# Optimization experiments

Hardware: AMD Instinct MI355X
Metric: run time of the kernel (lower is better)

Reference implementation:

```python
import jax, jax.numpy as jnp
import numpy as np

B, C, H, W, K, NH = 4, 128, 64, 64, 7, 8
DH = C // NH          # per-head dim
PAD = (K - 1) // 2    # symmetric padding since K is odd


def setup_inputs() -> dict:
    key = jax.random.key(0)
    ks = jax.random.split(key, 9)
    s = 1.0 / np.sqrt(C)
    f32 = jnp.float32
    return {
        "x": jax.random.normal(ks[0], (B, C, H, W), f32),
        "wq": jax.random.normal(ks[1], (C, C), f32) * s,
        "bq": jax.random.normal(ks[2], (C,), f32) * 0.01,
        "wk": jax.random.normal(ks[3], (C, C), f32) * s,
        "bk": jax.random.normal(ks[4], (C,), f32) * 0.01,
        "wv": jax.random.normal(ks[5], (C, C), f32) * s,
        "bv": jax.random.normal(ks[6], (C,), f32) * 0.01,
        "pos_h": jax.random.normal(ks[7], (NH, K), f32) * 0.02,
        "pos_w": jax.random.normal(ks[8], (NH, K), f32) * 0.02,
    }


def _unfold(p):
    # p: [B,C,H+K-1,W+K-1] -> [B,C,H,W,K,K] (KxK neighborhood per pixel),
    # matching torch .unfold(2,K,1).unfold(3,K,1). Loop is over fixed kernel size only.
    p1 = jnp.stack([p[:, :, i:i + H, :] for i in range(K)], axis=-1)      # [B,C,H,W+K-1,K]
    return jnp.stack([p1[:, :, :, j:j + W, :] for j in range(K)], axis=-1)  # [B,C,H,W,K,K]


def reference(x, wq, bq, wk, bk, wv, bv, pos_h, pos_w):
    cx = x  # cx defaults to x in the original module
    pc = jnp.pad(cx, ((0, 0), (0, 0), (PAD, PAD), (PAD, PAD)))
    # 1x1 convs are pointwise channel mixes
    k = jnp.einsum('oc,bchw->bohw', wk, pc) + bk[None, :, None, None]
    v = jnp.einsum('oc,bchw->bohw', wv, pc) + bv[None, :, None, None]
    q = jnp.einsum('oc,bchw->bohw', wq, x) + bq[None, :, None, None]

    ku = _unfold(k).reshape(B, NH, DH, H, W, K, K)
    vu = _unfold(v).reshape(B, NH, DH, H, W, K, K)
    qh = q.reshape(B, NH, DH, H, W)

    # per-pixel logits over KxK neighborhood
    logits = jnp.einsum('bndhw,bndhwij->bnhwij', qh, ku)  # [B,NH,H,W,K,K]
    logits = logits + pos_h[None, :, None, None, :, None] + pos_w[None, :, None, None, None, :]

    weights = jax.nn.softmax(logits.reshape(B, NH, H, W, K * K), axis=-1)
    out = jnp.einsum('bnhwk,bndhwk->bndhw', weights, vu.reshape(B, NH, DH, H, W, K * K))
    return out.reshape(B, C, H, W)
```

## Files before the change

### kernel.cpp

```cpp
#include <hip/hip_runtime.h>
#include <cmath>

constexpr int Bn = 4, Cn = 128, Hn = 64, Wn = 64, Kn = 7, NHn = 8, DHn = 16, PADn = 3;
constexpr int HWn = Hn * Wn;
constexpr int TS = 16;
constexpr int HALO = TS + Kn - 1;
constexpr int NPIX = HALO * HALO;
constexpr int PSTRIDE_U16 = 24;
constexpr int PSTRIDE_U32 = 12;

typedef float f32x4 __attribute__((ext_vector_type(4)));
typedef short short8 __attribute__((ext_vector_type(8)));
typedef unsigned int u32x4 __attribute__((ext_vector_type(4)));
typedef unsigned short u16x4 __attribute__((ext_vector_type(4)));
typedef unsigned short u16x8 __attribute__((ext_vector_type(8)));

__device__ __forceinline__ unsigned short f32_to_bf16_rne(float f) {
  unsigned u = __float_as_uint(f);
  unsigned r = u + 0x7fffu + ((u >> 16) & 1u);
  return (unsigned short)(r >> 16);
}
__device__ __forceinline__ float bf16_to_f32(unsigned short h) {
  return __uint_as_float(((unsigned)h) << 16);
}
__device__ __forceinline__ float bflo(unsigned u) { return __uint_as_float(u << 16); }
__device__ __forceinline__ float bfhi(unsigned u) { return __uint_as_float(u & 0xffff0000u); }

__global__ __launch_bounds__(256)
void prep(const float* __restrict__ x,
          const float* __restrict__ wq, const float* __restrict__ wk,
          const float* __restrict__ wv,
          unsigned short* __restrict__ Whl, unsigned short* __restrict__ xThl)
{
  const int t = threadIdx.x;
  if (blockIdx.z == 4) {
    if (blockIdx.y != 0 || blockIdx.x >= 48) return;
    const int mat = blockIdx.x >> 4;
    const int chunk = blockIdx.x & 15;
    const float* W = (mat == 0) ? wq : (mat == 1) ? wk : wv;
    const int i = (chunk * 256 + t) * 4;
    const f32x4 v = *reinterpret_cast<const f32x4*>(W + i);
    unsigned short h[4], l[4];
#pragma unroll
    for (int j = 0; j < 4; ++j) {
      h[j] = f32_to_bf16_rne(v[j]);
      l[j] = f32_to_bf16_rne(v[j] - bf16_to_f32(h[j]));
    }
    unsigned short* base = Whl + (size_t)mat * 2 * 16384;
    *reinterpret_cast<uint2*>(base + i) =
        make_uint2(h[0] | ((unsigned)h[1] << 16), h[2] | ((unsigned)h[3] << 16));
    *reinterpret_cast<uint2*>(base + 16384 + i) =
        make_uint2(l[0] | ((unsigned)l[1] << 16), l[2] | ((unsigned)l[3] << 16));
    return;
  }

  __shared__ float sm[32][65];
  const int b   = blockIdx.z;
  const int c0g = blockIdx.y * 32;
  const int p0g = blockIdx.x * 64;
  const float* xb = x + (size_t)b * Cn * HWn;

#pragma unroll
  for (int rep = 0; rep < 2; ++rep) {
    const int cl = rep * 16 + (t >> 4);
    const int pl = (t & 15) * 4;
    const f32x4 v = *reinterpret_cast<const f32x4*>(xb + (size_t)(c0g + cl) * HWn + p0g + pl);
    sm[cl][pl + 0] = v[0]; sm[cl][pl + 1] = v[1];
    sm[cl][pl + 2] = v[2]; sm[cl][pl + 3] = v[3];
  }
  __syncthreads();

  const int pl = t >> 2;
  const int c0 = (t & 3) * 8;
  u32x4 hw, lw;
#pragma unroll
  for (int j = 0; j < 4; ++j) {
    const float v0 = sm[c0 + 2 * j][pl];
    const float v1 = sm[c0 + 2 * j + 1][pl];
    const unsigned short h0 = f32_to_bf16_rne(v0);
    const unsigned short h1 = f32_to_bf16_rne(v1);
    const unsigned short l0 = f32_to_bf16_rne(v0 - bf16_to_f32(h0));
    const unsigned short l1 = f32_to_bf16_rne(v1 - bf16_to_f32(h1));
    hw[j] = h0 | ((unsigned)h1 << 16);
    lw[j] = l0 | ((unsigned)l1 << 16);
  }
  unsigned short* dst = xThl + (size_t)b * 2 * HWn * Cn + (size_t)(p0g + pl) * Cn + c0g + c0;
  *reinterpret_cast<u32x4*>(dst)            = hw;
  *reinterpret_cast<u32x4*>(dst + HWn * Cn) = lw;
}

__global__ __launch_bounds__(64)
void qkv_mfma(const unsigned short* __restrict__ Whl,
              const unsigned short* __restrict__ xThl,
              const float* __restrict__ bq_, const float* __restrict__ bk_,
              const float* __restrict__ bv_,
              float* __restrict__ qo, unsigned short* __restrict__ kbf,
              unsigned short* __restrict__ vbf)
{
  const int z   = blockIdx.z;
  const int mat = z >> 2;
  const int b   = z & 3;
  const float* bias = (mat == 0) ? bq_ : (mat == 1) ? bk_ : bv_;

  const int lane = threadIdx.x;
  const int r    = lane & 15;
  const int quad = lane >> 4;
  const int mbase = blockIdx.y * 64;
  const int nbase = blockIdx.x * 64;

  const unsigned short* Wm = Whl  + (size_t)mat * 2 * Cn * Cn;
  const unsigned short* Xb = xThl + (size_t)b   * 2 * HWn * Cn;

  f32x4 acc[4][4] = {};

#pragma unroll
  for (int ks = 0; ks < 4; ++ks) {
    const int kk = ks * 32 + quad * 8;
    short8 Ah[4], Al[4], Bh[4], Bl[4];
#pragma unroll
    for (int mt = 0; mt < 4; ++mt) {
      const unsigned short* p = Wm + (size_t)(mbase + mt * 16 + r) * Cn + kk;
      Ah[mt] = *reinterpret_cast<const short8*>(p);
      Al[mt] = *reinterpret_cast<const short8*>(p + Cn * Cn);
    }
#pragma unroll
    for (int nt = 0; nt < 4; ++nt) {
      const unsigned short* p = Xb + (size_t)(nbase + nt * 16 + r) * Cn + kk;
      Bh[nt] = *reinterpret_cast<const short8*>(p);
      Bl[nt] = *reinterpret_cast<const short8*>(p + HWn * Cn);
    }
#pragma unroll
    for (int mt = 0; mt < 4; ++mt)
#pragma unroll
      for (int nt = 0; nt < 4; ++nt) {
        acc[mt][nt] = __builtin_amdgcn_mfma_f32_16x16x32_bf16(Ah[mt], Bh[nt], acc[mt][nt], 0, 0, 0);
        acc[mt][nt] = __builtin_amdgcn_mfma_f32_16x16x32_bf16(Ah[mt], Bl[nt], acc[mt][nt], 0, 0, 0);
        acc[mt][nt] = __builtin_amdgcn_mfma_f32_16x16x32_bf16(Al[mt], Bh[nt], acc[mt][nt], 0, 0, 0);
      }
  }

#pragma unroll
  for (int mt = 0; mt < 4; ++mt) {
    const int n = blockIdx.y * 4 + mt;
    const f32x4 b4 = *reinterpret_cast<const f32x4*>(bias + mbase + mt * 16 + quad * 4);
#pragma unroll
    for (int nt = 0; nt < 4; ++nt) {
      const int p = nbase + nt * 16 + r;
      const size_t off = ((size_t)((b * NHn + n) * HWn + p)) * DHn + quad * 4;
      f32x4 val = acc[mt][nt] + b4;
      if (mat == 0) {
        *reinterpret_cast<f32x4*>(qo + off) = val;
      } else {
        unsigned short* y = (mat == 1) ? kbf : vbf;
        u16x4 pk;
        pk[0] = f32_to_bf16_rne(val[0]); pk[1] = f32_to_bf16_rne(val[1]);
        pk[2] = f32_to_bf16_rne(val[2]); pk[3] = f32_to_bf16_rne(val[3]);
        *reinterpret_cast<u16x4*>(y + off) = pk;
      }
    }
  }
}

__global__ __launch_bounds__(256)
void sasa_attn(const float* __restrict__ q, const unsigned short* __restrict__ kbf,
               const unsigned short* __restrict__ vbf, const float* __restrict__ bk_,
               const float* __restrict__ bv_, const float* __restrict__ pos_h,
               const float* __restrict__ pos_w, float* __restrict__ out)
{
  __shared__ __align__(16) unsigned short ksm[NPIX * PSTRIDE_U16];
  __shared__ __align__(16) unsigned short vsm[NPIX * PSTRIDE_U16];

  const int z  = blockIdx.z;
  const int b  = z >> 3;
  const int n  = z & 7;
  const int h0 = blockIdx.y * TS;
  const int w0 = blockIdx.x * TS;
  const int tid = threadIdx.x;
  const int tx = tid & 15;
  const int ty = tid >> 4;
  const int cbase = n * DHn;

  const unsigned short* kb = kbf + ((size_t)(b * NHn + n) * HWn) * DHn;
  const unsigned short* vb = vbf + ((size_t)(b * NHn + n) * HWn) * DHn;

  u16x8 kb0, kb1, vb0, vb1;
#pragma unroll
  for (int j = 0; j < 8; ++j) {
    kb0[j] = f32_to_bf16_rne(bk_[cbase + j]);
    kb1[j] = f32_to_bf16_rne(bk_[cbase + 8 + j]);
    vb0[j] = f32_to_bf16_rne(bv_[cbase + j]);
    vb1[j] = f32_to_bf16_rne(bv_[cbase + 8 + j]);
  }

  for (int c = tid; c < NPIX * 2; c += 256) {
    const int pix  = c >> 1;
    const int half = c & 1;
    const int hh = pix / HALO;
    const int ww = pix - hh * HALO;
    const int gh = h0 + hh - PADn;
    const int gw = w0 + ww - PADn;
    const bool inb = (gh >= 0) && (gh < Hn) && (gw >= 0) && (gw < Wn);
    u16x8 kd, vd;
    if (inb) {
      const size_t src = ((size_t)(gh * Wn + gw)) * DHn + half * 8;
      kd = *reinterpret_cast<const u16x8*>(kb + src);
      vd = *reinterpret_cast<const u16x8*>(vb + src);
    } else {
      kd = half ? kb1 : kb0;
      vd = half ? vb1 : vb0;
    }
    const int dst = pix * PSTRIDE_U16 + half * 8;
    *reinterpret_cast<u16x8*>(ksm + dst) = kd;
    *reinterpret_cast<u16x8*>(vsm + dst) = vd;
  }

  const int h = h0 + ty, w = w0 + tx;
  const int p = h * Wn + w;
  const float* qp = q + ((size_t)(b * NHn + n) * HWn + p) * DHn;
  float qr[DHn];
#pragma unroll
  for (int j = 0; j < 4; ++j) {
    const f32x4 t4 = *reinterpret_cast<const f32x4*>(qp + j * 4);
    qr[j * 4 + 0] = t4[0]; qr[j * 4 + 1] = t4[1];
    qr[j * 4 + 2] = t4[2]; qr[j * 4 + 3] = t4[3];
  }

  __syncthreads();

  const unsigned* ksu = reinterpret_cast<const unsigned*>(ksm);
  const unsigned* vsu = reinterpret_cast<const unsigned*>(vsm);

  float logits[Kn * Kn];
#pragma unroll
  for (int i = 0; i < Kn; ++i) {
    const float ph = pos_h[n * Kn + i];
#pragma unroll
    for (int j = 0; j < Kn; ++j) {
      const int base = ((ty + i) * HALO + (tx + j)) * PSTRIDE_U32;
      const u32x4 a = *reinterpret_cast<const u32x4*>(ksu + base);
      const u32x4 c = *reinterpret_cast<const u32x4*>(ksu + base + 4);
      float acc = qr[0] * bflo(a[0]);
      acc = fmaf(qr[1],  bfhi(a[0]), acc);
      acc = fmaf(qr[2],  bflo(a[1]), acc);  acc = fmaf(qr[3],  bfhi(a[1]), acc);
      acc = fmaf(qr[4],  bflo(a[2]), acc);  acc = fmaf(qr[5],  bfhi(a[2]), acc);
      acc = fmaf(qr[6],  bflo(a[3]), acc);  acc = fmaf(qr[7],  bfhi(a[3]), acc);
      acc = fmaf(qr[8],  bflo(c[0]), acc);  acc = fmaf(qr[9],  bfhi(c[0]), acc);
      acc = fmaf(qr[10], bflo(c[1]), acc);  acc = fmaf(qr[11], bfhi(c[1]), acc);
      acc = fmaf(qr[12], bflo(c[2]), acc);  acc = fmaf(qr[13], bfhi(c[2]), acc);
      acc = fmaf(qr[14], bflo(c[3]), acc);  acc = fmaf(qr[15], bfhi(c[3]), acc);
      logits[i * Kn + j] = acc + ph + pos_w[n * Kn + j];
    }
  }

  float mx = -1e30f;
#pragma unroll
  for (int t = 0; t < Kn * Kn; ++t) mx = fmaxf(mx, logits[t]);
  float sum = 0.0f;
#pragma unroll
  for (int t = 0; t < Kn * Kn; ++t) {
    const float e = __expf(logits[t] - mx);
    logits[t] = e;
    sum += e;
  }
  const float inv = 1.0f / sum;

  float o[DHn] = {};
#pragma unroll
  for (int i = 0; i < Kn; ++i) {
#pragma unroll
    for (int j = 0; j < Kn; ++j) {
      const float wt = logits[i * Kn + j];
      const int base = ((ty + i) * HALO + (tx + j)) * PSTRIDE_U32;
      const u32x4 a = *reinterpret_cast<const u32x4*>(vsu + base);
      const u32x4 c = *reinterpret_cast<const u32x4*>(vsu + base + 4);
      o[0]  = fmaf(wt, bflo(a[0]), o[0]);   o[1]  = fmaf(wt, bfhi(a[0]), o[1]);
      o[2]  = fmaf(wt, bflo(a[1]), o[2]);   o[3]  = fmaf(wt, bfhi(a[1]), o[3]);
      o[4]  = fmaf(wt, bflo(a[2]), o[4]);   o[5]  = fmaf(wt, bfhi(a[2]), o[5]);
      o[6]  = fmaf(wt, bflo(a[3]), o[6]);   o[7]  = fmaf(wt, bfhi(a[3]), o[7]);
      o[8]  = fmaf(wt, bflo(c[0]), o[8]);   o[9]  = fmaf(wt, bfhi(c[0]), o[9]);
      o[10] = fmaf(wt, bflo(c[1]), o[10]);  o[11] = fmaf(wt, bfhi(c[1]), o[11]);
      o[12] = fmaf(wt, bflo(c[2]), o[12]);  o[13] = fmaf(wt, bfhi(c[2]), o[13]);
      o[14] = fmaf(wt, bflo(c[3]), o[14]);  o[15] = fmaf(wt, bfhi(c[3]), o[15]);
    }
  }

  float* ob = out + ((size_t)(b * Cn + cbase)) * HWn + p;
#pragma unroll
  for (int d = 0; d < DHn; ++d) ob[(size_t)d * HWn] = o[d] * inv;
}

extern "C" void kernel_launch(void* const* d_in, const int* in_sizes, int n_in,
                              void* d_out, int out_size, void* d_ws, size_t ws_size,
                              hipStream_t stream) {
  const float* x     = (const float*)d_in[0];
  const float* wq    = (const float*)d_in[1];
  const float* bq    = (const float*)d_in[2];
  const float* wk    = (const float*)d_in[3];
  const float* bk    = (const float*)d_in[4];
  const float* wv    = (const float*)d_in[5];
  const float* bv    = (const float*)d_in[6];
  const float* pos_h = (const float*)d_in[7];
  const float* pos_w = (const float*)d_in[8];
  float* out = (float*)d_out;

  const size_t tensor_elems = (size_t)Bn * Cn * HWn;
  float*          q    = (float*)d_ws;
  unsigned short* kbf  = (unsigned short*)(q + tensor_elems);
  unsigned short* vbf  = kbf + tensor_elems;
  unsigned short* Whl  = vbf + tensor_elems;
  unsigned short* xThl = Whl + (size_t)3 * 2 * Cn * Cn;

  dim3 gp(HWn / 64, Cn / 32, Bn + 1);
  prep<<<gp, 256, 0, stream>>>(x, wq, wk, wv, Whl, xThl);

  dim3 g1(HWn / 64, Cn / 64, 3 * Bn);
  qkv_mfma<<<g1, 64, 0, stream>>>(Whl, xThl, bq, bk, bv, q, kbf, vbf);

  dim3 g2(Wn / TS, Hn / TS, Bn * NHn);
  sasa_attn<<<g2, 256, 0, stream>>>(q, kbf, vbf, bk, bv, pos_h, pos_w, out);
}
```

Measured before the change: 111.5 us.

## Compute neighborhood attention logits and weighted sum with MFMA instructions

Rewrites the attention kernel so each wavefront processes a 16-pixel row segment and computes the 7x7 neighborhood logits and the value aggregation with bf16 16x16x32 MFMA, using a banded 16-wide window with masked positional bias. Q is now stored as split bf16 hi/lo planes so the MFMA dot product keeps near-fp32 query precision, and V is transposed into a channel-major packed LDS layout to act as the B operand. This replaces many scalar FMAs per pixel with matrix instructions, at the cost of redundant work on masked window entries and bf16 rounding of the softmax weights.

```diff
diff --git a/kernel.cpp b/kernel.cpp
--- a/kernel.cpp
+++ b/kernel.cpp
@@ -4,10 +4,12 @@
 constexpr int Bn = 4, Cn = 128, Hn = 64, Wn = 64, Kn = 7, NHn = 8, DHn = 16, PADn = 3;
 constexpr int HWn = Hn * Wn;
 constexpr int TS = 16;
-constexpr int HALO = TS + Kn - 1;
-constexpr int NPIX = HALO * HALO;
-constexpr int PSTRIDE_U16 = 24;
-constexpr int PSTRIDE_U32 = 12;
+constexpr size_t QPLANE = (size_t)Bn * NHn * HWn * DHn;
+
+constexpr int HR = 22;
+constexpr int HC = 24;
+constexpr int KP = 24;
+constexpr int VW = 14;
 
 typedef float f32x4 __attribute__((ext_vector_type(4)));
 typedef short short8 __attribute__((ext_vector_type(8)));
@@ -23,8 +25,16 @@
 __device__ __forceinline__ float bf16_to_f32(unsigned short h) {
   return __uint_as_float(((unsigned)h) << 16);
 }
-__device__ __forceinline__ float bflo(unsigned u) { return __uint_as_float(u << 16); }
-__device__ __forceinline__ float bfhi(unsigned u) { return __uint_as_float(u & 0xffff0000u); }
+__device__ __forceinline__ unsigned pk_bf16(float lo, float hi) {
+  return (__float_as_uint(lo) >> 16) | (__float_as_uint(hi) & 0xffff0000u);
+}
+__device__ __forceinline__ f32x4 max4(f32x4 a, f32x4 b) {
+  a[0] = fmaxf(a[0], b[0]); a[1] = fmaxf(a[1], b[1]);
+  a[2] = fmaxf(a[2], b[2]); a[3] = fmaxf(a[3], b[3]);
+  return a;
+}
+
+union UVcast { u32x4 u; short8 s; };
 
 __global__ __launch_bounds__(256)
 void prep(const float* __restrict__ x,
@@ -94,7 +104,7 @@
               const unsigned short* __restrict__ xThl,
               const float* __restrict__ bq_, const float* __restrict__ bk_,
               const float* __restrict__ bv_,
-              float* __restrict__ qo, unsigned short* __restrict__ kbf,
+              unsigned short* __restrict__ qo, unsigned short* __restrict__ kbf,
               unsigned short* __restrict__ vbf)
 {
   const int z   = blockIdx.z;
@@ -149,39 +159,54 @@
       const size_t off = ((size_t)((b * NHn + n) * HWn + p)) * DHn + quad * 4;
       f32x4 val = acc[mt][nt] + b4;
       if (mat == 0) {
-        *reinterpret_cast<f32x4*>(qo + off) = val;
+        u16x4 hi4, lo4;
+#pragma unroll
+        for (int j = 0; j < 4; ++j) {
+          const unsigned short hb = f32_to_bf16_rne(val[j]);
+          hi4[j] = hb;
+          lo4[j] = f32_to_bf16_rne(val[j] - bf16_to_f32(hb));
+        }
+        *reinterpret_cast<u16x4*>(qo + off)          = hi4;
+        *reinterpret_cast<u16x4*>(qo + QPLANE + off) = lo4;
       } else {
         unsigned short* y = (mat == 1) ? kbf : vbf;
-        u16x4 pk;
-        pk[0] = f32_to_bf16_rne(val[0]); pk[1] = f32_to_bf16_rne(val[1]);
-        pk[2] = f32_to_bf16_rne(val[2]); pk[3] = f32_to_bf16_rne(val[3]);
-        *reinterpret_cast<u16x4*>(y + off) = pk;
+        u16x4 pkv;
+        pkv[0] = f32_to_bf16_rne(val[0]); pkv[1] = f32_to_bf16_rne(val[1]);
+        pkv[2] = f32_to_bf16_rne(val[2]); pkv[3] = f32_to_bf16_rne(val[3]);
+        *reinterpret_cast<u16x4*>(y + off) = pkv;
       }
     }
   }
 }
 
 __global__ __launch_bounds__(256)
-void sasa_attn(const float* __restrict__ q, const unsigned short* __restrict__ kbf,
-               const unsigned short* __restrict__ vbf, const float* __restrict__ bk_,
-               const float* __restrict__ bv_, const float* __restrict__ pos_h,
-               const float* __restrict__ pos_w, float* __restrict__ out)
+void sasa_attn(const unsigned short* __restrict__ qhl,
+               const unsigned short* __restrict__ kbf,
+               const unsigned short* __restrict__ vbf,
+               const float* __restrict__ bk_, const float* __restrict__ bv_,
+               const float* __restrict__ pos_h, const float* __restrict__ pos_w,
+               float* __restrict__ out)
 {
-  __shared__ __align__(16) unsigned short ksm[NPIX * PSTRIDE_U16];
-  __shared__ __align__(16) unsigned short vsm[NPIX * PSTRIDE_U16];
+  __shared__ __align__(16) unsigned short ksm[HR * HC * KP];
+  __shared__ __align__(16) unsigned       vsm[HR * DHn * VW];
 
   const int z  = blockIdx.z;
   const int b  = z >> 3;
   const int n  = z & 7;
   const int h0 = blockIdx.y * TS;
   const int w0 = blockIdx.x * TS;
-  const int tid = threadIdx.x;
-  const int tx = tid & 15;
-  const int ty = tid >> 4;
+  const int tid  = threadIdx.x;
+  const int lane = tid & 63;
+  const int wv   = tid >> 6;
+  const int r    = lane & 15;
+  const int quad = lane >> 4;
   const int cbase = n * DHn;
 
   const unsigned short* kb = kbf + ((size_t)(b * NHn + n) * HWn) * DHn;
   const unsigned short* vb = vbf + ((size_t)(b * NHn + n) * HWn) * DHn;
+  const size_t qbase = ((size_t)(b * NHn + n) * HWn) * DHn;
+  const unsigned short* qhp = qhl + qbase;
+  const unsigned short* qlp = qhl + QPLANE + qbase;
 
   u16x8 kb0, kb1, vb0, vb1;
 #pragma unroll
@@ -192,101 +217,141 @@
     vb1[j] = f32_to_bf16_rne(bv_[cbase + 8 + j]);
   }
 
-  for (int c = tid; c < NPIX * 2; c += 256) {
+  for (int c = tid; c < HR * HC * 2; c += 256) {
     const int pix  = c >> 1;
     const int half = c & 1;
-    const int hh = pix / HALO;
-    const int ww = pix - hh * HALO;
+    const int hh = pix / HC;
+    const int ww = pix - hh * HC;
     const int gh = h0 + hh - PADn;
     const int gw = w0 + ww - PADn;
     const bool inb = (gh >= 0) && (gh < Hn) && (gw >= 0) && (gw < Wn);
-    u16x8 kd, vd;
-    if (inb) {
-      const size_t src = ((size_t)(gh * Wn + gw)) * DHn + half * 8;
-      kd = *reinterpret_cast<const u16x8*>(kb + src);
-      vd = *reinterpret_cast<const u16x8*>(vb + src);
-    } else {
-      kd = half ? kb1 : kb0;
-      vd = half ? vb1 : vb0;
-    }
-    const int dst = pix * PSTRIDE_U16 + half * 8;
-    *reinterpret_cast<u16x8*>(ksm + dst) = kd;
-    *reinterpret_cast<u16x8*>(vsm + dst) = vd;
-  }
-
-  const int h = h0 + ty, w = w0 + tx;
-  const int p = h * Wn + w;
-  const float* qp = q + ((size_t)(b * NHn + n) * HWn + p) * DHn;
-  float qr[DHn];
-#pragma unroll
-  for (int j = 0; j < 4; ++j) {
-    const f32x4 t4 = *reinterpret_cast<const f32x4*>(qp + j * 4);
-    qr[j * 4 + 0] = t4[0]; qr[j * 4 + 1] = t4[1];
-    qr[j * 4 + 2] = t4[2]; qr[j * 4 + 3] = t4[3];
+    u16x8 kd;
+    if (inb) kd = *reinterpret_cast<const u16x8*>(kb + ((size_t)(gh * Wn + gw)) * DHn + half * 8);
+    else     kd = half ? kb1 : kb0;
+    *reinterpret_cast<u16x8*>(ksm + pix * KP + half * 8) = kd;
+  }
+
+  for (int pp = tid; pp < HR * (HC / 2); pp += 256) {
+    const int hh = pp / (HC / 2);
+    const int wp = pp - hh * (HC / 2);
+    const int gh = h0 + hh - PADn;
+    u16x8 a0, a1, c0, c1;
+    {
+      const int gw = w0 + 2 * wp - PADn;
+      const bool inb = (gh >= 0) && (gh < Hn) && (gw >= 0) && (gw < Wn);
+      if (inb) {
+        const size_t src = ((size_t)(gh * Wn + gw)) * DHn;
+        a0 = *reinterpret_cast<const u16x8*>(vb + src);
+        a1 = *reinterpret_cast<const u16x8*>(vb + src + 8);
+      } else { a0 = vb0; a1 = vb1; }
+    }
+    {
+      const int gw = w0 + 2 * wp + 1 - PADn;
+      const bool inb = (gh >= 0) && (gh < Hn) && (gw >= 0) && (gw < Wn);
+      if (inb) {
+        const size_t src = ((size_t)(gh * Wn + gw)) * DHn;
+        c0 = *reinterpret_cast<const u16x8*>(vb + src);
+        c1 = *reinterpret_cast<const u16x8*>(vb + src + 8);
+      } else { c0 = vb0; c1 = vb1; }
+    }
+    unsigned* dst = vsm + (hh * DHn) * VW + wp;
+#pragma unroll
+    for (int d = 0; d < 8; ++d)
+      dst[d * VW] = (unsigned)(unsigned short)a0[d] | ((unsigned)(unsigned short)c0[d] << 16);
+#pragma unroll
+    for (int d = 0; d < 8; ++d)
+      dst[(8 + d) * VW] = (unsigned)(unsigned short)a1[d] | ((unsigned)(unsigned short)c1[d] << 16);
+  }
+
+  float ph[7];
+#pragma unroll
+  for (int i = 0; i < 7; ++i) ph[i] = pos_h[n * Kn + i];
+  f32x4 pw4[2];
+#pragma unroll
+  for (int win = 0; win < 2; ++win) {
+#pragma unroll
+    for (int reg = 0; reg < 4; ++reg) {
+      const int ww = win * 8 + 4 * quad + reg;
+      const int j  = ww - r;
+      const bool valid = (j >= 0) && (j < 7) && (win == 0 || ww >= 16);
+      const int jc = j < 0 ? 0 : (j > 6 ? 6 : j);
+      const float pv = pos_w[n * Kn + jc];
+      pw4[win][reg] = valid ? pv : -1e30f;
+    }
   }
 
   __syncthreads();
 
-  const unsigned* ksu = reinterpret_cast<const unsigned*>(ksm);
-  const unsigned* vsu = reinterpret_cast<const unsigned*>(vsm);
-
-  float logits[Kn * Kn];
-#pragma unroll
-  for (int i = 0; i < Kn; ++i) {
-    const float ph = pos_h[n * Kn + i];
-#pragma unroll
-    for (int j = 0; j < Kn; ++j) {
-      const int base = ((ty + i) * HALO + (tx + j)) * PSTRIDE_U32;
-      const u32x4 a = *reinterpret_cast<const u32x4*>(ksu + base);
-      const u32x4 c = *reinterpret_cast<const u32x4*>(ksu + base + 4);
-      float acc = qr[0] * bflo(a[0]);
-      acc = fmaf(qr[1],  bfhi(a[0]), acc);
-      acc = fmaf(qr[2],  bflo(a[1]), acc);  acc = fmaf(qr[3],  bfhi(a[1]), acc);
-      acc = fmaf(qr[4],  bflo(a[2]), acc);  acc = fmaf(qr[5],  bfhi(a[2]), acc);
-      acc = fmaf(qr[6],  bflo(a[3]), acc);  acc = fmaf(qr[7],  bfhi(a[3]), acc);
-      acc = fmaf(qr[8],  bflo(c[0]), acc);  acc = fmaf(qr[9],  bfhi(c[0]), acc);
-      acc = fmaf(qr[10], bflo(c[1]), acc);  acc = fmaf(qr[11], bfhi(c[1]), acc);
-      acc = fmaf(qr[12], bflo(c[2]), acc);  acc = fmaf(qr[13], bfhi(c[2]), acc);
-      acc = fmaf(qr[14], bflo(c[3]), acc);  acc = fmaf(qr[15], bfhi(c[3]), acc);
-      logits[i * Kn + j] = acc + ph + pos_w[n * Kn + j];
-    }
-  }
-
-  float mx = -1e30f;
-#pragma unroll
-  for (int t = 0; t < Kn * Kn; ++t) mx = fmaxf(mx, logits[t]);
-  float sum = 0.0f;
-#pragma unroll
-  for (int t = 0; t < Kn * Kn; ++t) {
-    const float e = __expf(logits[t] - mx);
-    logits[t] = e;
-    sum += e;
-  }
-  const float inv = 1.0f / sum;
-
-  float o[DHn] = {};
-#pragma unroll
-  for (int i = 0; i < Kn; ++i) {
-#pragma unroll
-    for (int j = 0; j < Kn; ++j) {
-      const float wt = logits[i * Kn + j];
-      const int base = ((ty + i) * HALO + (tx + j)) * PSTRIDE_U32;
-      const u32x4 a = *reinterpret_cast<const u32x4*>(vsu + base);
-      const u32x4 c = *reinterpret_cast<const u32x4*>(vsu + base + 4);
-      o[0]  = fmaf(wt, bflo(a[0]), o[0]);   o[1]  = fmaf(wt, bfhi(a[0]), o[1]);
-      o[2]  = fmaf(wt, bflo(a[1]), o[2]);   o[3]  = fmaf(wt, bfhi(a[1]), o[3]);
-      o[4]  = fmaf(wt, bflo(a[2]), o[4]);   o[5]  = fmaf(wt, bfhi(a[2]), o[5]);
-      o[6]  = fmaf(wt, bflo(a[3]), o[6]);   o[7]  = fmaf(wt, bfhi(a[3]), o[7]);
-      o[8]  = fmaf(wt, bflo(c[0]), o[8]);   o[9]  = fmaf(wt, bfhi(c[0]), o[9]);
-      o[10] = fmaf(wt, bflo(c[1]), o[10]);  o[11] = fmaf(wt, bfhi(c[1]), o[11]);
-      o[12] = fmaf(wt, bflo(c[2]), o[12]);  o[13] = fmaf(wt, bfhi(c[2]), o[13]);
-      o[14] = fmaf(wt, bflo(c[3]), o[14]);  o[15] = fmaf(wt, bfhi(c[3]), o[15]);
-    }
-  }
-
-  float* ob = out + ((size_t)(b * Cn + cbase)) * HWn + p;
-#pragma unroll
-  for (int d = 0; d < DHn; ++d) ob[(size_t)d * HWn] = o[d] * inv;
+  const f32x4 zero4 = {};
+  for (int hl = 0; hl < 4; ++hl) {
+    const int h = wv * 4 + hl;
+
+    const int pix = (h0 + h) * Wn + (w0 + r);
+    const unsigned short* qsel = (quad < 2) ? qhp : qlp;
+    const short8 qf = *reinterpret_cast<const short8*>(qsel + (size_t)pix * DHn + (quad & 1) * 8);
+
+    f32x4 L[14];
+#pragma unroll
+    for (int i = 0; i < 7; ++i) {
+#pragma unroll
+      for (int win = 0; win < 2; ++win) {
+        const short8 kf = *reinterpret_cast<const short8*>(
+            ksm + ((h + i) * HC + win * 8 + r) * KP + (quad & 1) * 8);
+        f32x4 d = __builtin_amdgcn_mfma_f32_16x16x32_bf16(kf, qf, zero4, 0, 0, 0);
+        d = d + pw4[win];
+        d = d + (f32x4)ph[i];
+        L[i * 2 + win] = d;
+      }
+    }
+
+    f32x4 M4 = L[0];
+#pragma unroll
+    for (int t = 1; t < 14; ++t) M4 = max4(M4, L[t]);
+    float m = fmaxf(fmaxf(M4[0], M4[1]), fmaxf(M4[2], M4[3]));
+    m = fmaxf(m, __shfl_xor(m, 16, 64));
+    m = fmaxf(m, __shfl_xor(m, 32, 64));
+
+    f32x4 S4 = {};
+#pragma unroll
+    for (int t = 0; t < 14; ++t) {
+      f32x4 e;
+      e[0] = __expf(L[t][0] - m);
+      e[1] = __expf(L[t][1] - m);
+      e[2] = __expf(L[t][2] - m);
+      e[3] = __expf(L[t][3] - m);
+      L[t] = e;
+      S4 += e;
+    }
+    float s = (S4[0] + S4[1]) + (S4[2] + S4[3]);
+    s += __shfl_xor(s, 16, 64);
+    s += __shfl_xor(s, 32, 64);
+    const float inv = 1.0f / s;
+
+    f32x4 oA = {}, oB = {};
+#pragma unroll
+    for (int i = 0; i < 7; ++i) {
+      const f32x4 e0 = L[2 * i]     * (f32x4)inv;
+      const f32x4 e1 = L[2 * i + 1] * (f32x4)inv;
+      UVcast A;
+      A.u[0] = pk_bf16(e0[0], e0[1]);
+      A.u[1] = pk_bf16(e0[2], e0[3]);
+      A.u[2] = pk_bf16(e1[0], e1[1]);
+      A.u[3] = pk_bf16(e1[2], e1[3]);
+
+      const unsigned* vp = vsm + ((h + i) * DHn + r) * VW + 2 * quad;
+      const uint2 v0 = *reinterpret_cast<const uint2*>(vp);
+      const uint2 v1 = *reinterpret_cast<const uint2*>(vp + 4);
+      UVcast Bv;
+      Bv.u[0] = v0.x; Bv.u[1] = v0.y; Bv.u[2] = v1.x; Bv.u[3] = v1.y;
+
+      f32x4& acc = (i & 1) ? oB : oA;
+      acc = __builtin_amdgcn_mfma_f32_16x16x32_bf16(A.s, Bv.s, acc, 0, 0, 0);
+    }
+    const f32x4 O = oA + oB;
+
+    float* op = out + ((size_t)(b * Cn + cbase + r)) * HWn + (h0 + h) * Wn + w0 + 4 * quad;
+    *reinterpret_cast<f32x4*>(op) = O;
+  }
 }
 
 extern "C" void kernel_launch(void* const* d_in, const int* in_sizes, int n_in,
@@ -304,8 +369,8 @@
   float* out = (float*)d_out;
 
   const size_t tensor_elems = (size_t)Bn * Cn * HWn;
-  float*          q    = (float*)d_ws;
-  unsigned short* kbf  = (unsigned short*)(q + tensor_elems);
+  unsigned short* qhl  = (unsigned short*)d_ws;
+  unsigned short* kbf  = qhl + 2 * tensor_elems;
   unsigned short* vbf  = kbf + tensor_elems;
   unsigned short* Whl  = vbf + tensor_elems;
   unsigned short* xThl = Whl + (size_t)3 * 2 * Cn * Cn;
@@ -314,8 +379,8 @@
   prep<<<gp, 256, 0, stream>>>(x, wq, wk, wv, Whl, xThl);
 
   dim3 g1(HWn / 64, Cn / 64, 3 * Bn);
-  qkv_mfma<<<g1, 64, 0, stream>>>(Whl, xThl, bq, bk, bv, q, kbf, vbf);
+  qkv_mfma<<<g1, 64, 0, stream>>>(Whl, xThl, bq, bk, bv, qhl, kbf, vbf);
 
   dim3 g2(Wn / TS, Hn / TS, Bn * NHn);
-  sasa_attn<<<g2, 256, 0, stream>>>(q, kbf, vbf, bk, bv, pos_h, pos_w, out);
-}
+  sasa_attn<<<g2, 256, 0, stream>>>(qhl, kbf, vbf, bk, bv, pos_h, pos_w, out);
+}
```

Result: no change. 111.5 us (+0.0%).
